# Performance work log

Measured on AMD Instinct MI355X. Metric: run time of the kernel, lower is better.

## Reference

```python
import jax, jax.numpy as jnp
import numpy as np

COMMITMENT_COST = 0.25
NUM_EMBEDDINGS = 8192
EMBED_DIM = 64


def setup_inputs() -> dict:
    key = jax.random.key(0)
    k1, k2 = jax.random.split(key)
    inputs = jax.random.normal(k1, (16, 32, 32, EMBED_DIM), dtype=jnp.float32)
    # nn.init.uniform_(-1/K, 1/K)
    codebook = jax.random.uniform(
        k2, (NUM_EMBEDDINGS, EMBED_DIM), dtype=jnp.float32,
        minval=-1.0 / NUM_EMBEDDINGS, maxval=1.0 / NUM_EMBEDDINGS)
    return {"inputs": inputs, "codebook": codebook}


def reference(inputs, codebook):
    D = codebook.shape[-1]
    flat = inputs.reshape(-1, D)  # [N, D]
    # Squared euclidean distances (same argmin as torch.cdist).
    d2 = (jnp.sum(flat * flat, axis=1, keepdims=True)
          - 2.0 * flat @ codebook.T
          + jnp.sum(codebook * codebook, axis=1))  # [N, K]
    idx = jnp.argmin(d2, axis=1)  # [N]
    # one-hot @ codebook == direct gather
    quantized = codebook[idx].reshape(inputs.shape)
    sg = jax.lax.stop_gradient
    e_latent = (sg(quantized) - inputs) ** 2
    q_latent = (quantized - sg(inputs)) ** 2
    loss = q_latent + COMMITMENT_COST * e_latent
    quantized_st = inputs + sg(quantized - inputs)  # straight-through
    return (loss, quantized_st)
```

## Files before the change

### kernel.cpp

```cpp
#include <hip/hip_runtime.h>
#include <float.h>

#define NROWS 16384
#define KC 8192
#define DIM 64
#define BM 128
#define KSPLIT 4
#define CPS (KC / KSPLIT)
#define TILE 256
#define NTILES (CPS / TILE)

typedef __attribute__((ext_vector_type(8))) short bf16x8;
typedef __attribute__((ext_vector_type(4))) float f32x4;

#define WS_CB16 0
#define WS_X16  (KC * DIM * 2)
#define WS_GMIN (WS_X16 + NROWS * DIM * 2)

__device__ inline unsigned short f2bf(float f) {
    union { float f; unsigned u; } v; v.f = f;
    unsigned u = v.u;
    unsigned r = u + 0x7FFFu + ((u >> 16) & 1u);
    return (unsigned short)(r >> 16);
}
__device__ inline unsigned asu(float f) { union { float f; unsigned u; } v; v.f = f; return v.u; }
__device__ inline float asf(unsigned u) { union { float f; unsigned u; } v; v.u = u; return v.f; }

__global__ __launch_bounds__(256) void vq_prep(
        const float* __restrict__ x, const float* __restrict__ cb,
        unsigned short* __restrict__ x16, unsigned short* __restrict__ cb16,
        unsigned* __restrict__ gmin) {
    const int bx = blockIdx.x;
    const int tid = threadIdx.x;
    if (bx < 512) {
        const int g = bx * 256 + tid;
        const float4* s = (const float4*)x + (size_t)g * 2;
        float4 a = s[0], b = s[1];
        bf16x8 o;
        o[0] = (short)f2bf(-a.x); o[1] = (short)f2bf(-a.y);
        o[2] = (short)f2bf(-a.z); o[3] = (short)f2bf(-a.w);
        o[4] = (short)f2bf(-b.x); o[5] = (short)f2bf(-b.y);
        o[6] = (short)f2bf(-b.z); o[7] = (short)f2bf(-b.w);
        ((bf16x8*)x16)[g] = o;
        if (g < NROWS) gmin[g] = 0xFFFFFFFFu;
    } else {
        const int g = (bx - 512) * 256 + tid;
        const float4* s = (const float4*)cb + (size_t)g * 2;
        float4 a = s[0], b = s[1];
        bf16x8 o;
        o[0] = (short)f2bf(a.x); o[1] = (short)f2bf(a.y);
        o[2] = (short)f2bf(a.z); o[3] = (short)f2bf(a.w);
        o[4] = (short)f2bf(b.x); o[5] = (short)f2bf(b.y);
        o[6] = (short)f2bf(b.z); o[7] = (short)f2bf(b.w);
        ((bf16x8*)cb16)[g] = o;
    }
}

__global__ __launch_bounds__(256, 2) void vq_main(
        const unsigned short* __restrict__ x16,
        const unsigned short* __restrict__ cb16,
        unsigned* __restrict__ gmin) {
    __shared__ __attribute__((aligned(16))) char smem[2][32768];

    const int tid = threadIdx.x;
    const int lane = tid & 63;
    const int wave = tid >> 6;
    const int waveM = wave >> 1, waveN = wave & 1;
    const int quad = lane >> 4, c15 = lane & 15;

    const int rowTile = blockIdx.x & 127;
    const int split = blockIdx.x >> 7;
    const int splitBase = split * CPS;
    const size_t rowBase = (size_t)rowTile * BM;

    unsigned srcOff[8], dstOff[8];
#pragma unroll
    for (int j = 0; j < 8; ++j) {
        int p = j * 256 + tid;
        int q = (p & ~7) | ((p & 7) ^ ((p >> 3) & 7));
        srcOff[j] = (unsigned)q * 16u;
        dstOff[j] = (unsigned)(j * 256 + wave * 64) * 16u;
    }
    const char* gcb = (const char*)cb16 + (size_t)splitBase * DIM * 2;

#pragma unroll
    for (int j = 0; j < 8; ++j)
        __builtin_amdgcn_global_load_lds(
            (const __attribute__((address_space(1))) void*)(gcb + srcOff[j]),
            (__attribute__((address_space(3))) void*)(&smem[0][0] + dstOff[j]),
            16, 0, 0);

    bf16x8 afr[4][2];
#pragma unroll
    for (int fm = 0; fm < 4; ++fm) {
        const unsigned short* xr = x16 + (rowBase + waveM * 64 + fm * 16 + c15) * DIM;
#pragma unroll
        for (int kk = 0; kk < 2; ++kk)
            afr[fm][kk] = *(const bf16x8*)(xr + kk * 32 + quad * 8);
    }

    float key[4][4];
#pragma unroll
    for (int a = 0; a < 4; ++a)
#pragma unroll
        for (int b = 0; b < 4; ++b) key[a][b] = FLT_MAX;
    unsigned slotReg[2][4];
#pragma unroll
    for (int h = 0; h < 2; ++h)
#pragma unroll
        for (int fnl = 0; fnl < 4; ++fnl)
            slotReg[h][fnl] = (unsigned)(splitBase + waveN * 128 + h * 64 +
                                         fnl * 16 + c15);
    const f32x4 Z = {0.f, 0.f, 0.f, 0.f};

    __syncthreads();

    for (int t = 0; t < NTILES; ++t) {
        const int buf = t & 1;
        if (t + 1 < NTILES) {
            const char* gn = gcb + (size_t)(t + 1) * TILE * DIM * 2;
            char* lb = &smem[buf ^ 1][0];
#pragma unroll
            for (int j = 0; j < 8; ++j)
                __builtin_amdgcn_global_load_lds(
                    (const __attribute__((address_space(1))) void*)(gn + srcOff[j]),
                    (__attribute__((address_space(3))) void*)(lb + dstOff[j]),
                    16, 0, 0);
        }

        const bf16x8* B16 = (const bf16x8*)&smem[buf][0];
#pragma unroll
        for (int h = 0; h < 2; ++h) {
            bf16x8 bfr[4][2];
#pragma unroll
            for (int fnl = 0; fnl < 4; ++fnl) {
                int rB = waveN * 128 + h * 64 + fnl * 16 + c15;
#pragma unroll
                for (int kk = 0; kk < 2; ++kk) {
                    int cch = kk * 4 + quad;
                    bfr[fnl][kk] = B16[rB * 8 + (cch ^ (rB & 7))];
                }
            }
            f32x4 acc[4][4];
#pragma unroll
            for (int fm = 0; fm < 4; ++fm)
#pragma unroll
                for (int fnl = 0; fnl < 4; ++fnl) {
                    f32x4 t0 = __builtin_amdgcn_mfma_f32_16x16x32_bf16(
                        afr[fm][0], bfr[fnl][0], Z, 0, 0, 0);
                    acc[fm][fnl] = __builtin_amdgcn_mfma_f32_16x16x32_bf16(
                        afr[fm][1], bfr[fnl][1], t0, 0, 0, 0);
                }
#pragma unroll
            for (int fm = 0; fm < 4; ++fm)
#pragma unroll
                for (int rg = 0; rg < 4; ++rg) {
                    unsigned u0 = (asu(acc[fm][0][rg]) & 0xFFFFE000u) | slotReg[h][0];
                    unsigned u1 = (asu(acc[fm][1][rg]) & 0xFFFFE000u) | slotReg[h][1];
                    unsigned u2 = (asu(acc[fm][2][rg]) & 0xFFFFE000u) | slotReg[h][2];
                    unsigned u3 = (asu(acc[fm][3][rg]) & 0xFFFFE000u) | slotReg[h][3];
                    float k = key[fm][rg];
                    k = fminf(k, fminf(asf(u0), asf(u1)));
                    k = fminf(k, fminf(asf(u2), asf(u3)));
                    key[fm][rg] = k;
                }
        }
#pragma unroll
        for (int h = 0; h < 2; ++h)
#pragma unroll
            for (int fnl = 0; fnl < 4; ++fnl) slotReg[h][fnl] += TILE;
        __syncthreads();
    }

#pragma unroll
    for (int fm = 0; fm < 4; ++fm)
#pragma unroll
        for (int rg = 0; rg < 4; ++rg) {
            float k = key[fm][rg];
            k = fminf(k, __shfl_xor(k, 1));
            k = fminf(k, __shfl_xor(k, 2));
            k = fminf(k, __shfl_xor(k, 4));
            k = fminf(k, __shfl_xor(k, 8));
            key[fm][rg] = k;
        }
    if (c15 == 0) {
#pragma unroll
        for (int fm = 0; fm < 4; ++fm)
#pragma unroll
            for (int rg = 0; rg < 4; ++rg) {
                unsigned u = asu(key[fm][rg]);
                unsigned m = (u & 0x80000000u) ? ~u : (u | 0x80000000u);
                atomicMin(&gmin[rowBase + waveM * 64 + fm * 16 + quad * 4 + rg], m);
            }
    }
}

__global__ __launch_bounds__(256) void vq_out(
        const float* __restrict__ x, const float* __restrict__ cb,
        const unsigned* __restrict__ gmin,
        float* __restrict__ out_loss, float* __restrict__ out_q) {
    __shared__ int idxs[16];
    const int tid = threadIdx.x;
    const size_t row0 = (size_t)blockIdx.x * 16;
    if (tid < 16) {
        unsigned u = gmin[row0 + tid];
        unsigned b = (u & 0x80000000u) ? (u ^ 0x80000000u) : ~u;
        idxs[tid] = (int)(b & 8191u);
    }
    __syncthreads();
    const int r = tid >> 4;
    const int d4 = tid & 15;
    const int code = idxs[r];
    float4 q4 = ((const float4*)(cb + (size_t)code * DIM))[d4];
    float4 x4 = ((const float4*)(x + (row0 + r) * DIM))[d4];
    float4 l4;
    l4.x = 1.25f * (q4.x - x4.x) * (q4.x - x4.x);
    l4.y = 1.25f * (q4.y - x4.y) * (q4.y - x4.y);
    l4.z = 1.25f * (q4.z - x4.z) * (q4.z - x4.z);
    l4.w = 1.25f * (q4.w - x4.w) * (q4.w - x4.w);
    ((float4*)out_loss)[(row0 + r) * 16 + d4] = l4;
    ((float4*)out_q)[(row0 + r) * 16 + d4] = q4;
}

extern "C" void kernel_launch(void* const* d_in, const int* in_sizes, int n_in,
                              void* d_out, int out_size, void* d_ws, size_t ws_size,
                              hipStream_t stream) {
    const float* x = (const float*)d_in[0];
    const float* cb = (const float*)d_in[1];
    char* ws = (char*)d_ws;
    unsigned short* cb16 = (unsigned short*)(ws + WS_CB16);
    unsigned short* x16 = (unsigned short*)(ws + WS_X16);
    unsigned* gmin = (unsigned*)(ws + WS_GMIN);

    float* out_loss = (float*)d_out;
    float* out_q = out_loss + (size_t)NROWS * DIM;

    vq_prep<<<768, 256, 0, stream>>>(x, cb, x16, cb16, gmin);
    vq_main<<<(NROWS / BM) * KSPLIT, 256, 0, stream>>>(x16, cb16, gmin);
    vq_out<<<NROWS / 16, 256, 0, stream>>>(x, cb, gmin, out_loss, out_q);
}
```

Before: 87.16 us.

## Fuse output gather into main kernel via last-block ticket and retile rows

Removes the separate output kernel: each row tile's split blocks atomically bump a counter, and the last arriving block reads the final argmin and writes loss and quantized outputs. Row tile shrinks to 64 and K-split drops to 2, so there are still 512 blocks, but each reuses a codebook tile over fewer rows. An in-block shared-memory reduction across the two N-waves now comes before the global atomicMin. This saves one kernel launch and a gmin round trip, but halves MFMA work per LDS codebook load and adds fences and atomics.

```diff
diff --git a/kernel.cpp b/kernel.cpp
--- a/kernel.cpp
+++ b/kernel.cpp
@@ -4,11 +4,12 @@
 #define NROWS 16384
 #define KC 8192
 #define DIM 64
-#define BM 128
-#define KSPLIT 4
+#define BM 64
+#define KSPLIT 2
 #define CPS (KC / KSPLIT)
 #define TILE 256
 #define NTILES (CPS / TILE)
+#define NRT (NROWS / BM)
 
 typedef __attribute__((ext_vector_type(8))) short bf16x8;
 typedef __attribute__((ext_vector_type(4))) float f32x4;
@@ -16,6 +17,7 @@
 #define WS_CB16 0
 #define WS_X16  (KC * DIM * 2)
 #define WS_GMIN (WS_X16 + NROWS * DIM * 2)
+#define WS_CNT  (WS_GMIN + NROWS * 4)
 
 __device__ inline unsigned short f2bf(float f) {
     union { float f; unsigned u; } v; v.f = f;
@@ -29,7 +31,7 @@
 __global__ __launch_bounds__(256) void vq_prep(
         const float* __restrict__ x, const float* __restrict__ cb,
         unsigned short* __restrict__ x16, unsigned short* __restrict__ cb16,
-        unsigned* __restrict__ gmin) {
+        unsigned* __restrict__ gmin, unsigned* __restrict__ cnt) {
     const int bx = blockIdx.x;
     const int tid = threadIdx.x;
     if (bx < 512) {
@@ -43,6 +45,7 @@
         o[6] = (short)f2bf(-b.z); o[7] = (short)f2bf(-b.w);
         ((bf16x8*)x16)[g] = o;
         if (g < NROWS) gmin[g] = 0xFFFFFFFFu;
+        if (g < NRT) cnt[g] = 0u;
     } else {
         const int g = (bx - 512) * 256 + tid;
         const float4* s = (const float4*)cb + (size_t)g * 2;
@@ -59,8 +62,13 @@
 __global__ __launch_bounds__(256, 2) void vq_main(
         const unsigned short* __restrict__ x16,
         const unsigned short* __restrict__ cb16,
-        unsigned* __restrict__ gmin) {
+        const float* __restrict__ x, const float* __restrict__ cb,
+        unsigned* __restrict__ gmin, unsigned* __restrict__ cnt,
+        float* __restrict__ out_loss, float* __restrict__ out_q) {
     __shared__ __attribute__((aligned(16))) char smem[2][32768];
+    __shared__ float redK[BM][2];
+    __shared__ int idxs[BM];
+    __shared__ int ticket;
 
     const int tid = threadIdx.x;
     const int lane = tid & 63;
@@ -68,8 +76,8 @@
     const int waveM = wave >> 1, waveN = wave & 1;
     const int quad = lane >> 4, c15 = lane & 15;
 
-    const int rowTile = blockIdx.x & 127;
-    const int split = blockIdx.x >> 7;
+    const int rowTile = blockIdx.x >> 1;
+    const int split = blockIdx.x & 1;
     const int splitBase = split * CPS;
     const size_t rowBase = (size_t)rowTile * BM;
 
@@ -90,18 +98,18 @@
             (__attribute__((address_space(3))) void*)(&smem[0][0] + dstOff[j]),
             16, 0, 0);
 
-    bf16x8 afr[4][2];
-#pragma unroll
-    for (int fm = 0; fm < 4; ++fm) {
-        const unsigned short* xr = x16 + (rowBase + waveM * 64 + fm * 16 + c15) * DIM;
+    bf16x8 afr[2][2];
+#pragma unroll
+    for (int fm = 0; fm < 2; ++fm) {
+        const unsigned short* xr = x16 + (rowBase + waveM * 32 + fm * 16 + c15) * DIM;
 #pragma unroll
         for (int kk = 0; kk < 2; ++kk)
             afr[fm][kk] = *(const bf16x8*)(xr + kk * 32 + quad * 8);
     }
 
-    float key[4][4];
-#pragma unroll
-    for (int a = 0; a < 4; ++a)
+    float key[2][4];
+#pragma unroll
+    for (int a = 0; a < 2; ++a)
 #pragma unroll
         for (int b = 0; b < 4; ++b) key[a][b] = FLT_MAX;
     unsigned slotReg[2][4];
@@ -141,9 +149,9 @@
                     bfr[fnl][kk] = B16[rB * 8 + (cch ^ (rB & 7))];
                 }
             }
-            f32x4 acc[4][4];
-#pragma unroll
-            for (int fm = 0; fm < 4; ++fm)
+            f32x4 acc[2][4];
+#pragma unroll
+            for (int fm = 0; fm < 2; ++fm)
 #pragma unroll
                 for (int fnl = 0; fnl < 4; ++fnl) {
                     f32x4 t0 = __builtin_amdgcn_mfma_f32_16x16x32_bf16(
@@ -152,7 +160,7 @@
                         afr[fm][1], bfr[fnl][1], t0, 0, 0, 0);
                 }
 #pragma unroll
-            for (int fm = 0; fm < 4; ++fm)
+            for (int fm = 0; fm < 2; ++fm)
 #pragma unroll
                 for (int rg = 0; rg < 4; ++rg) {
                     unsigned u0 = (asu(acc[fm][0][rg]) & 0xFFFFE000u) | slotReg[h][0];
@@ -173,7 +181,7 @@
     }
 
 #pragma unroll
-    for (int fm = 0; fm < 4; ++fm)
+    for (int fm = 0; fm < 2; ++fm)
 #pragma unroll
         for (int rg = 0; rg < 4; ++rg) {
             float k = key[fm][rg];
@@ -185,41 +193,49 @@
         }
     if (c15 == 0) {
 #pragma unroll
-        for (int fm = 0; fm < 4; ++fm)
-#pragma unroll
-            for (int rg = 0; rg < 4; ++rg) {
-                unsigned u = asu(key[fm][rg]);
-                unsigned m = (u & 0x80000000u) ? ~u : (u | 0x80000000u);
-                atomicMin(&gmin[rowBase + waveM * 64 + fm * 16 + quad * 4 + rg], m);
-            }
-    }
-}
-
-__global__ __launch_bounds__(256) void vq_out(
-        const float* __restrict__ x, const float* __restrict__ cb,
-        const unsigned* __restrict__ gmin,
-        float* __restrict__ out_loss, float* __restrict__ out_q) {
-    __shared__ int idxs[16];
-    const int tid = threadIdx.x;
-    const size_t row0 = (size_t)blockIdx.x * 16;
-    if (tid < 16) {
-        unsigned u = gmin[row0 + tid];
-        unsigned b = (u & 0x80000000u) ? (u ^ 0x80000000u) : ~u;
-        idxs[tid] = (int)(b & 8191u);
-    }
-    __syncthreads();
-    const int r = tid >> 4;
-    const int d4 = tid & 15;
-    const int code = idxs[r];
-    float4 q4 = ((const float4*)(cb + (size_t)code * DIM))[d4];
-    float4 x4 = ((const float4*)(x + (row0 + r) * DIM))[d4];
-    float4 l4;
-    l4.x = 1.25f * (q4.x - x4.x) * (q4.x - x4.x);
-    l4.y = 1.25f * (q4.y - x4.y) * (q4.y - x4.y);
-    l4.z = 1.25f * (q4.z - x4.z) * (q4.z - x4.z);
-    l4.w = 1.25f * (q4.w - x4.w) * (q4.w - x4.w);
-    ((float4*)out_loss)[(row0 + r) * 16 + d4] = l4;
-    ((float4*)out_q)[(row0 + r) * 16 + d4] = q4;
+        for (int fm = 0; fm < 2; ++fm)
+#pragma unroll
+            for (int rg = 0; rg < 4; ++rg)
+                redK[waveM * 32 + fm * 16 + quad * 4 + rg][waveN] = key[fm][rg];
+    }
+    __syncthreads();
+
+    if (tid < BM) {
+        float m = fminf(redK[tid][0], redK[tid][1]);
+        unsigned u = asu(m);
+        unsigned mp = (u & 0x80000000u) ? ~u : (u | 0x80000000u);
+        atomicMin(&gmin[rowBase + tid], mp);
+    }
+    __threadfence();
+    __syncthreads();
+    if (tid == 0) ticket = (int)atomicAdd(&cnt[rowTile], 1u);
+    __syncthreads();
+
+    if (ticket == KSPLIT - 1) {
+        __threadfence();
+        if (tid < BM) {
+            unsigned mm = atomicMin(&gmin[rowBase + tid], 0xFFFFFFFFu);
+            unsigned b = (mm & 0x80000000u) ? (mm ^ 0x80000000u) : ~mm;
+            idxs[tid] = (int)(b & 8191u);
+        }
+        __syncthreads();
+#pragma unroll
+        for (int j = 0; j < 4; ++j) {
+            int e = j * 256 + tid;
+            int r = e >> 4;
+            int d4 = e & 15;
+            int code = idxs[r];
+            float4 q4 = ((const float4*)(cb + (size_t)code * DIM))[d4];
+            float4 x4 = ((const float4*)(x + (rowBase + r) * DIM))[d4];
+            float4 l4;
+            l4.x = 1.25f * (q4.x - x4.x) * (q4.x - x4.x);
+            l4.y = 1.25f * (q4.y - x4.y) * (q4.y - x4.y);
+            l4.z = 1.25f * (q4.z - x4.z) * (q4.z - x4.z);
+            l4.w = 1.25f * (q4.w - x4.w) * (q4.w - x4.w);
+            ((float4*)out_loss)[(rowBase + r) * 16 + d4] = l4;
+            ((float4*)out_q)[(rowBase + r) * 16 + d4] = q4;
+        }
+    }
 }
 
 extern "C" void kernel_launch(void* const* d_in, const int* in_sizes, int n_in,
@@ -231,11 +247,12 @@
     unsigned short* cb16 = (unsigned short*)(ws + WS_CB16);
     unsigned short* x16 = (unsigned short*)(ws + WS_X16);
     unsigned* gmin = (unsigned*)(ws + WS_GMIN);
+    unsigned* cnt = (unsigned*)(ws + WS_CNT);
 
     float* out_loss = (float*)d_out;
     float* out_q = out_loss + (size_t)NROWS * DIM;
 
-    vq_prep<<<768, 256, 0, stream>>>(x, cb, x16, cb16, gmin);
-    vq_main<<<(NROWS / BM) * KSPLIT, 256, 0, stream>>>(x16, cb16, gmin);
-    vq_out<<<NROWS / 16, 256, 0, stream>>>(x, cb, gmin, out_loss, out_q);
-}
+    vq_prep<<<768, 256, 0, stream>>>(x, cb, x16, cb16, gmin, cnt);
+    vq_main<<<NRT * KSPLIT, 256, 0, stream>>>(x16, cb16, x, cb, gmin, cnt,
+                                              out_loss, out_q);
+}
```

Measured after the change: 134.6 us. 54.4% more time.

## Fuse prep, distance-argmin and output into one cooperative kernel with grid syncs

Applied to the files above, without the earlier changes.

Merges the three kernels into a single cooperative launch of 512 blocks that runs conversion, the MFMA distance/argmin, and the gather/loss phases separated by grid-wide syncs, with a fallback to three launches if the cooperative launch fails. To fit two blocks per CU with 32KB LDS, the codebook tile shrinks from 256 to 128 rows, and the block-to-tile mapping is interleaved across splits. The aim is to remove launch gaps between kernels. In exchange, grid.sync adds barrier cost, the smaller tile doubles loop iterations and syncthreads, and the output phase runs on fewer blocks.

```diff
diff --git a/kernel.cpp b/kernel.cpp
--- a/kernel.cpp
+++ b/kernel.cpp
@@ -1,5 +1,8 @@
 #include <hip/hip_runtime.h>
+#include <hip/hip_cooperative_groups.h>
 #include <float.h>
+
+namespace cg = cooperative_groups;
 
 #define NROWS 16384
 #define KC 8192
@@ -7,8 +10,9 @@
 #define BM 128
 #define KSPLIT 4
 #define CPS (KC / KSPLIT)
-#define TILE 256
+#define TILE 128
 #define NTILES (CPS / TILE)
+#define GRID 512
 
 typedef __attribute__((ext_vector_type(8))) short bf16x8;
 typedef __attribute__((ext_vector_type(4))) float f32x4;
@@ -26,14 +30,12 @@
 __device__ inline unsigned asu(float f) { union { float f; unsigned u; } v; v.f = f; return v.u; }
 __device__ inline float asf(unsigned u) { union { float f; unsigned u; } v; v.u = u; return v.f; }
 
-__global__ __launch_bounds__(256) void vq_prep(
+__device__ __forceinline__ void phaseA(int bx, int tid,
         const float* __restrict__ x, const float* __restrict__ cb,
         unsigned short* __restrict__ x16, unsigned short* __restrict__ cb16,
         unsigned* __restrict__ gmin) {
-    const int bx = blockIdx.x;
-    const int tid = threadIdx.x;
-    if (bx < 512) {
-        const int g = bx * 256 + tid;
+    const int g = bx * 256 + tid;
+    {
         const float4* s = (const float4*)x + (size_t)g * 2;
         float4 a = s[0], b = s[1];
         bf16x8 o;
@@ -42,9 +44,8 @@
         o[4] = (short)f2bf(-b.x); o[5] = (short)f2bf(-b.y);
         o[6] = (short)f2bf(-b.z); o[7] = (short)f2bf(-b.w);
         ((bf16x8*)x16)[g] = o;
-        if (g < NROWS) gmin[g] = 0xFFFFFFFFu;
-    } else {
-        const int g = (bx - 512) * 256 + tid;
+    }
+    if (g < KC * DIM / 8) {
         const float4* s = (const float4*)cb + (size_t)g * 2;
         float4 a = s[0], b = s[1];
         bf16x8 o;
@@ -54,28 +55,26 @@
         o[6] = (short)f2bf(b.z); o[7] = (short)f2bf(b.w);
         ((bf16x8*)cb16)[g] = o;
     }
-}
-
-__global__ __launch_bounds__(256, 2) void vq_main(
+    if (g < NROWS) gmin[g] = 0xFFFFFFFFu;
+}
+
+__device__ __forceinline__ void phaseB(int bx, int tid, char* smem,
         const unsigned short* __restrict__ x16,
         const unsigned short* __restrict__ cb16,
         unsigned* __restrict__ gmin) {
-    __shared__ __attribute__((aligned(16))) char smem[2][32768];
-
-    const int tid = threadIdx.x;
     const int lane = tid & 63;
     const int wave = tid >> 6;
     const int waveM = wave >> 1, waveN = wave & 1;
     const int quad = lane >> 4, c15 = lane & 15;
 
-    const int rowTile = blockIdx.x & 127;
-    const int split = blockIdx.x >> 7;
+    const int rowTile = bx >> 2;
+    const int split = bx & 3;
     const int splitBase = split * CPS;
     const size_t rowBase = (size_t)rowTile * BM;
 
-    unsigned srcOff[8], dstOff[8];
-#pragma unroll
-    for (int j = 0; j < 8; ++j) {
+    unsigned srcOff[4], dstOff[4];
+#pragma unroll
+    for (int j = 0; j < 4; ++j) {
         int p = j * 256 + tid;
         int q = (p & ~7) | ((p & 7) ^ ((p >> 3) & 7));
         srcOff[j] = (unsigned)q * 16u;
@@ -84,10 +83,10 @@
     const char* gcb = (const char*)cb16 + (size_t)splitBase * DIM * 2;
 
 #pragma unroll
-    for (int j = 0; j < 8; ++j)
+    for (int j = 0; j < 4; ++j)
         __builtin_amdgcn_global_load_lds(
             (const __attribute__((address_space(1))) void*)(gcb + srcOff[j]),
-            (__attribute__((address_space(3))) void*)(&smem[0][0] + dstOff[j]),
+            (__attribute__((address_space(3))) void*)(smem + dstOff[j]),
             16, 0, 0);
 
     bf16x8 afr[4][2];
@@ -104,13 +103,10 @@
     for (int a = 0; a < 4; ++a)
 #pragma unroll
         for (int b = 0; b < 4; ++b) key[a][b] = FLT_MAX;
-    unsigned slotReg[2][4];
-#pragma unroll
-    for (int h = 0; h < 2; ++h)
-#pragma unroll
-        for (int fnl = 0; fnl < 4; ++fnl)
-            slotReg[h][fnl] = (unsigned)(splitBase + waveN * 128 + h * 64 +
-                                         fnl * 16 + c15);
+    unsigned slotReg[4];
+#pragma unroll
+    for (int fnl = 0; fnl < 4; ++fnl)
+        slotReg[fnl] = (unsigned)(splitBase + waveN * 64 + fnl * 16 + c15);
     const f32x4 Z = {0.f, 0.f, 0.f, 0.f};
 
     __syncthreads();
@@ -119,56 +115,51 @@
         const int buf = t & 1;
         if (t + 1 < NTILES) {
             const char* gn = gcb + (size_t)(t + 1) * TILE * DIM * 2;
-            char* lb = &smem[buf ^ 1][0];
-#pragma unroll
-            for (int j = 0; j < 8; ++j)
+            char* lb = smem + (buf ^ 1) * 16384;
+#pragma unroll
+            for (int j = 0; j < 4; ++j)
                 __builtin_amdgcn_global_load_lds(
                     (const __attribute__((address_space(1))) void*)(gn + srcOff[j]),
                     (__attribute__((address_space(3))) void*)(lb + dstOff[j]),
                     16, 0, 0);
         }
 
-        const bf16x8* B16 = (const bf16x8*)&smem[buf][0];
-#pragma unroll
-        for (int h = 0; h < 2; ++h) {
-            bf16x8 bfr[4][2];
+        const bf16x8* B16 = (const bf16x8*)(smem + buf * 16384);
+        bf16x8 bfr[4][2];
+#pragma unroll
+        for (int fnl = 0; fnl < 4; ++fnl) {
+            int rB = waveN * 64 + fnl * 16 + c15;
+#pragma unroll
+            for (int kk = 0; kk < 2; ++kk) {
+                int cch = kk * 4 + quad;
+                bfr[fnl][kk] = B16[rB * 8 + (cch ^ (rB & 7))];
+            }
+        }
+        f32x4 acc[4][4];
+#pragma unroll
+        for (int fm = 0; fm < 4; ++fm)
 #pragma unroll
             for (int fnl = 0; fnl < 4; ++fnl) {
-                int rB = waveN * 128 + h * 64 + fnl * 16 + c15;
-#pragma unroll
-                for (int kk = 0; kk < 2; ++kk) {
-                    int cch = kk * 4 + quad;
-                    bfr[fnl][kk] = B16[rB * 8 + (cch ^ (rB & 7))];
-                }
-            }
-            f32x4 acc[4][4];
-#pragma unroll
-            for (int fm = 0; fm < 4; ++fm)
-#pragma unroll
-                for (int fnl = 0; fnl < 4; ++fnl) {
-                    f32x4 t0 = __builtin_amdgcn_mfma_f32_16x16x32_bf16(
-                        afr[fm][0], bfr[fnl][0], Z, 0, 0, 0);
-                    acc[fm][fnl] = __builtin_amdgcn_mfma_f32_16x16x32_bf16(
-                        afr[fm][1], bfr[fnl][1], t0, 0, 0, 0);
-                }
-#pragma unroll
-            for (int fm = 0; fm < 4; ++fm)
-#pragma unroll
-                for (int rg = 0; rg < 4; ++rg) {
-                    unsigned u0 = (asu(acc[fm][0][rg]) & 0xFFFFE000u) | slotReg[h][0];
-                    unsigned u1 = (asu(acc[fm][1][rg]) & 0xFFFFE000u) | slotReg[h][1];
-                    unsigned u2 = (asu(acc[fm][2][rg]) & 0xFFFFE000u) | slotReg[h][2];
-                    unsigned u3 = (asu(acc[fm][3][rg]) & 0xFFFFE000u) | slotReg[h][3];
-                    float k = key[fm][rg];
-                    k = fminf(k, fminf(asf(u0), asf(u1)));
-                    k = fminf(k, fminf(asf(u2), asf(u3)));
-                    key[fm][rg] = k;
-                }
-        }
-#pragma unroll
-        for (int h = 0; h < 2; ++h)
-#pragma unroll
-            for (int fnl = 0; fnl < 4; ++fnl) slotReg[h][fnl] += TILE;
+                f32x4 t0 = __builtin_amdgcn_mfma_f32_16x16x32_bf16(
+                    afr[fm][0], bfr[fnl][0], Z, 0, 0, 0);
+                acc[fm][fnl] = __builtin_amdgcn_mfma_f32_16x16x32_bf16(
+                    afr[fm][1], bfr[fnl][1], t0, 0, 0, 0);
+            }
+#pragma unroll
+        for (int fm = 0; fm < 4; ++fm)
+#pragma unroll
+            for (int rg = 0; rg < 4; ++rg) {
+                unsigned u0 = (asu(acc[fm][0][rg]) & 0xFFFFE000u) | slotReg[0];
+                unsigned u1 = (asu(acc[fm][1][rg]) & 0xFFFFE000u) | slotReg[1];
+                unsigned u2 = (asu(acc[fm][2][rg]) & 0xFFFFE000u) | slotReg[2];
+                unsigned u3 = (asu(acc[fm][3][rg]) & 0xFFFFE000u) | slotReg[3];
+                float k = key[fm][rg];
+                k = fminf(k, fminf(asf(u0), asf(u1)));
+                k = fminf(k, fminf(asf(u2), asf(u3)));
+                key[fm][rg] = k;
+            }
+#pragma unroll
+        for (int fnl = 0; fnl < 4; ++fnl) slotReg[fnl] += TILE;
         __syncthreads();
     }
 
@@ -195,31 +186,70 @@
     }
 }
 
-__global__ __launch_bounds__(256) void vq_out(
+__device__ __forceinline__ void phaseC(int bx, int tid, char* smem,
         const float* __restrict__ x, const float* __restrict__ cb,
         const unsigned* __restrict__ gmin,
         float* __restrict__ out_loss, float* __restrict__ out_q) {
-    __shared__ int idxs[16];
-    const int tid = threadIdx.x;
-    const size_t row0 = (size_t)blockIdx.x * 16;
-    if (tid < 16) {
+    int* idxs = (int*)smem;
+    const size_t row0 = (size_t)bx * 32;
+    if (tid < 32) {
         unsigned u = gmin[row0 + tid];
         unsigned b = (u & 0x80000000u) ? (u ^ 0x80000000u) : ~u;
         idxs[tid] = (int)(b & 8191u);
     }
     __syncthreads();
-    const int r = tid >> 4;
-    const int d4 = tid & 15;
-    const int code = idxs[r];
-    float4 q4 = ((const float4*)(cb + (size_t)code * DIM))[d4];
-    float4 x4 = ((const float4*)(x + (row0 + r) * DIM))[d4];
-    float4 l4;
-    l4.x = 1.25f * (q4.x - x4.x) * (q4.x - x4.x);
-    l4.y = 1.25f * (q4.y - x4.y) * (q4.y - x4.y);
-    l4.z = 1.25f * (q4.z - x4.z) * (q4.z - x4.z);
-    l4.w = 1.25f * (q4.w - x4.w) * (q4.w - x4.w);
-    ((float4*)out_loss)[(row0 + r) * 16 + d4] = l4;
-    ((float4*)out_q)[(row0 + r) * 16 + d4] = q4;
+#pragma unroll
+    for (int j = 0; j < 2; ++j) {
+        int e = j * 256 + tid;
+        int r = e >> 4;
+        int d4 = e & 15;
+        int code = idxs[r];
+        float4 q4 = ((const float4*)(cb + (size_t)code * DIM))[d4];
+        float4 x4 = ((const float4*)(x + (row0 + r) * DIM))[d4];
+        float4 l4;
+        l4.x = 1.25f * (q4.x - x4.x) * (q4.x - x4.x);
+        l4.y = 1.25f * (q4.y - x4.y) * (q4.y - x4.y);
+        l4.z = 1.25f * (q4.z - x4.z) * (q4.z - x4.z);
+        l4.w = 1.25f * (q4.w - x4.w) * (q4.w - x4.w);
+        ((float4*)out_loss)[(row0 + r) * 16 + d4] = l4;
+        ((float4*)out_q)[(row0 + r) * 16 + d4] = q4;
+    }
+}
+
+__global__ __launch_bounds__(256, 2) void vq_all(
+        const float* __restrict__ x, const float* __restrict__ cb,
+        unsigned short* __restrict__ x16, unsigned short* __restrict__ cb16,
+        unsigned* __restrict__ gmin,
+        float* __restrict__ out_loss, float* __restrict__ out_q) {
+    __shared__ __attribute__((aligned(16))) char smem[32768];
+    cg::grid_group grid = cg::this_grid();
+    const int bx = blockIdx.x, tid = threadIdx.x;
+
+    phaseA(bx, tid, x, cb, x16, cb16, gmin);
+    grid.sync();
+    phaseB(bx, tid, smem, x16, cb16, gmin);
+    grid.sync();
+    phaseC(bx, tid, smem, x, cb, gmin, out_loss, out_q);
+}
+
+__global__ __launch_bounds__(256) void vq_prepK(
+        const float* __restrict__ x, const float* __restrict__ cb,
+        unsigned short* __restrict__ x16, unsigned short* __restrict__ cb16,
+        unsigned* __restrict__ gmin) {
+    phaseA(blockIdx.x, threadIdx.x, x, cb, x16, cb16, gmin);
+}
+__global__ __launch_bounds__(256, 2) void vq_mainK(
+        const unsigned short* __restrict__ x16,
+        const unsigned short* __restrict__ cb16, unsigned* __restrict__ gmin) {
+    __shared__ __attribute__((aligned(16))) char smem[32768];
+    phaseB(blockIdx.x, threadIdx.x, smem, x16, cb16, gmin);
+}
+__global__ __launch_bounds__(256) void vq_outK(
+        const float* __restrict__ x, const float* __restrict__ cb,
+        const unsigned* __restrict__ gmin,
+        float* __restrict__ out_loss, float* __restrict__ out_q) {
+    __shared__ __attribute__((aligned(16))) char smem[256];
+    phaseC(blockIdx.x, threadIdx.x, smem, x, cb, gmin, out_loss, out_q);
 }
 
 extern "C" void kernel_launch(void* const* d_in, const int* in_sizes, int n_in,
@@ -235,7 +265,13 @@
     float* out_loss = (float*)d_out;
     float* out_q = out_loss + (size_t)NROWS * DIM;
 
-    vq_prep<<<768, 256, 0, stream>>>(x, cb, x16, cb16, gmin);
-    vq_main<<<(NROWS / BM) * KSPLIT, 256, 0, stream>>>(x16, cb16, gmin);
-    vq_out<<<NROWS / 16, 256, 0, stream>>>(x, cb, gmin, out_loss, out_q);
-}
+    void* args[] = {(void*)&x, (void*)&cb, (void*)&x16, (void*)&cb16,
+                    (void*)&gmin, (void*)&out_loss, (void*)&out_q};
+    hipError_t err = hipLaunchCooperativeKernel(
+        reinterpret_cast<void*>(vq_all), dim3(GRID), dim3(256), args, 0, stream);
+    if (err != hipSuccess) {
+        vq_prepK<<<GRID, 256, 0, stream>>>(x, cb, x16, cb16, gmin);
+        vq_mainK<<<GRID, 256, 0, stream>>>(x16, cb16, gmin);
+        vq_outK<<<GRID, 256, 0, stream>>>(x, cb, gmin, out_loss, out_q);
+    }
+}
```

Result: slower. 186.9 us (+114.5%).

## Pre-swizzle bf16 operands into MFMA fragment layout and drop LDS staging

Applied to the files above, without the earlier changes.

The prep kernel now writes x and the codebook in bf16 in an MFMA-fragment-major layout, so each lane loads its operand fragment with one coalesced 16-byte global load. The main kernel no longer stages codebook tiles through LDS with barriers. Instead each wave streams its own 1024 codes straight from global or L2 into registers, double-buffering fragments. The block index mapping is also changed so the four K-splits of a row tile run adjacently. This removes LDS traffic and __syncthreads, but each wave now reads its B fragments independently, so L2 traffic rises and global-load latency must be hidden by the register prefetch alone.

```diff
diff --git a/kernel.cpp b/kernel.cpp
--- a/kernel.cpp
+++ b/kernel.cpp
@@ -7,8 +7,9 @@
 #define BM 128
 #define KSPLIT 4
 #define CPS (KC / KSPLIT)
-#define TILE 256
-#define NTILES (CPS / TILE)
+#define NRT (NROWS / BM)
+#define GRID (NRT * KSPLIT)
+#define WITERS 16
 
 typedef __attribute__((ext_vector_type(8))) short bf16x8;
 typedef __attribute__((ext_vector_type(4))) float f32x4;
@@ -30,146 +31,114 @@
         const float* __restrict__ x, const float* __restrict__ cb,
         unsigned short* __restrict__ x16, unsigned short* __restrict__ cb16,
         unsigned* __restrict__ gmin) {
-    const int bx = blockIdx.x;
-    const int tid = threadIdx.x;
-    if (bx < 512) {
-        const int g = bx * 256 + tid;
-        const float4* s = (const float4*)x + (size_t)g * 2;
+    const int g = blockIdx.x * 256 + threadIdx.x;
+    {
+        const int r = g >> 3, p = g & 7;
+        const int kk = p >> 2, quad = p & 3;
+        const float4* s = (const float4*)(x + (size_t)r * DIM + kk * 32 + quad * 8);
         float4 a = s[0], b = s[1];
         bf16x8 o;
         o[0] = (short)f2bf(-a.x); o[1] = (short)f2bf(-a.y);
         o[2] = (short)f2bf(-a.z); o[3] = (short)f2bf(-a.w);
         o[4] = (short)f2bf(-b.x); o[5] = (short)f2bf(-b.y);
         o[6] = (short)f2bf(-b.z); o[7] = (short)f2bf(-b.w);
-        ((bf16x8*)x16)[g] = o;
-        if (g < NROWS) gmin[g] = 0xFFFFFFFFu;
-    } else {
-        const int g = (bx - 512) * 256 + tid;
-        const float4* s = (const float4*)cb + (size_t)g * 2;
+        const int dest = (((r >> 4) * 2 + kk) * 4 + quad) * 16 + (r & 15);
+        ((bf16x8*)x16)[dest] = o;
+    }
+    if (g < KC * DIM / 8) {
+        const int c = g >> 3, p = g & 7;
+        const int kk = p >> 2, quad = p & 3;
+        const float4* s = (const float4*)(cb + (size_t)c * DIM + kk * 32 + quad * 8);
         float4 a = s[0], b = s[1];
         bf16x8 o;
         o[0] = (short)f2bf(a.x); o[1] = (short)f2bf(a.y);
         o[2] = (short)f2bf(a.z); o[3] = (short)f2bf(a.w);
         o[4] = (short)f2bf(b.x); o[5] = (short)f2bf(b.y);
         o[6] = (short)f2bf(b.z); o[7] = (short)f2bf(b.w);
-        ((bf16x8*)cb16)[g] = o;
-    }
+        const int dest = (((c >> 4) * 2 + kk) * 4 + quad) * 16 + (c & 15);
+        ((bf16x8*)cb16)[dest] = o;
+    }
+    if (g < NROWS) gmin[g] = 0xFFFFFFFFu;
 }
 
 __global__ __launch_bounds__(256, 2) void vq_main(
         const unsigned short* __restrict__ x16,
         const unsigned short* __restrict__ cb16,
         unsigned* __restrict__ gmin) {
-    __shared__ __attribute__((aligned(16))) char smem[2][32768];
-
     const int tid = threadIdx.x;
     const int lane = tid & 63;
     const int wave = tid >> 6;
     const int waveM = wave >> 1, waveN = wave & 1;
     const int quad = lane >> 4, c15 = lane & 15;
 
-    const int rowTile = blockIdx.x & 127;
-    const int split = blockIdx.x >> 7;
+    const int rowTile = blockIdx.x >> 2;
+    const int split = blockIdx.x & 3;
     const int splitBase = split * CPS;
     const size_t rowBase = (size_t)rowTile * BM;
 
-    unsigned srcOff[8], dstOff[8];
-#pragma unroll
-    for (int j = 0; j < 8; ++j) {
-        int p = j * 256 + tid;
-        int q = (p & ~7) | ((p & 7) ^ ((p >> 3) & 7));
-        srcOff[j] = (unsigned)q * 16u;
-        dstOff[j] = (unsigned)(j * 256 + wave * 64) * 16u;
-    }
-    const char* gcb = (const char*)cb16 + (size_t)splitBase * DIM * 2;
-
-#pragma unroll
-    for (int j = 0; j < 8; ++j)
-        __builtin_amdgcn_global_load_lds(
-            (const __attribute__((address_space(1))) void*)(gcb + srcOff[j]),
-            (__attribute__((address_space(3))) void*)(&smem[0][0] + dstOff[j]),
-            16, 0, 0);
-
+    const bf16x8* X = (const bf16x8*)x16;
     bf16x8 afr[4][2];
 #pragma unroll
     for (int fm = 0; fm < 4; ++fm) {
-        const unsigned short* xr = x16 + (rowBase + waveM * 64 + fm * 16 + c15) * DIM;
+        const int rb = (int)(rowBase >> 4) + waveM * 4 + fm;
 #pragma unroll
         for (int kk = 0; kk < 2; ++kk)
-            afr[fm][kk] = *(const bf16x8*)(xr + kk * 32 + quad * 8);
-    }
+            afr[fm][kk] = X[(rb * 2 + kk) * 64 + lane];
+    }
+
+    const bf16x8* B = (const bf16x8*)cb16;
+    const int codeBase = splitBase + waveN * 1024;
+    const int cb0 = codeBase >> 4;
 
     float key[4][4];
 #pragma unroll
     for (int a = 0; a < 4; ++a)
 #pragma unroll
         for (int b = 0; b < 4; ++b) key[a][b] = FLT_MAX;
-    unsigned slotReg[2][4];
-#pragma unroll
-    for (int h = 0; h < 2; ++h)
-#pragma unroll
-        for (int fnl = 0; fnl < 4; ++fnl)
-            slotReg[h][fnl] = (unsigned)(splitBase + waveN * 128 + h * 64 +
-                                         fnl * 16 + c15);
     const f32x4 Z = {0.f, 0.f, 0.f, 0.f};
 
-    __syncthreads();
-
-    for (int t = 0; t < NTILES; ++t) {
-        const int buf = t & 1;
-        if (t + 1 < NTILES) {
-            const char* gn = gcb + (size_t)(t + 1) * TILE * DIM * 2;
-            char* lb = &smem[buf ^ 1][0];
-#pragma unroll
-            for (int j = 0; j < 8; ++j)
-                __builtin_amdgcn_global_load_lds(
-                    (const __attribute__((address_space(1))) void*)(gn + srcOff[j]),
-                    (__attribute__((address_space(3))) void*)(lb + dstOff[j]),
-                    16, 0, 0);
+    bf16x8 bfr[2][4][2];
+#pragma unroll
+    for (int fn = 0; fn < 4; ++fn)
+#pragma unroll
+        for (int kk = 0; kk < 2; ++kk)
+            bfr[0][fn][kk] = B[((cb0 + fn) * 2 + kk) * 64 + lane];
+
+#pragma unroll
+    for (int it = 0; it < WITERS; ++it) {
+        const int cur = it & 1;
+        if (it + 1 < WITERS) {
+            const int cbn = cb0 + (it + 1) * 4;
+#pragma unroll
+            for (int fn = 0; fn < 4; ++fn)
+#pragma unroll
+                for (int kk = 0; kk < 2; ++kk)
+                    bfr[cur ^ 1][fn][kk] = B[((cbn + fn) * 2 + kk) * 64 + lane];
         }
-
-        const bf16x8* B16 = (const bf16x8*)&smem[buf][0];
-#pragma unroll
-        for (int h = 0; h < 2; ++h) {
-            bf16x8 bfr[4][2];
-#pragma unroll
-            for (int fnl = 0; fnl < 4; ++fnl) {
-                int rB = waveN * 128 + h * 64 + fnl * 16 + c15;
-#pragma unroll
-                for (int kk = 0; kk < 2; ++kk) {
-                    int cch = kk * 4 + quad;
-                    bfr[fnl][kk] = B16[rB * 8 + (cch ^ (rB & 7))];
-                }
+        f32x4 acc[4][4];
+#pragma unroll
+        for (int fm = 0; fm < 4; ++fm)
+#pragma unroll
+            for (int fn = 0; fn < 4; ++fn) {
+                f32x4 t0 = __builtin_amdgcn_mfma_f32_16x16x32_bf16(
+                    afr[fm][0], bfr[cur][fn][0], Z, 0, 0, 0);
+                acc[fm][fn] = __builtin_amdgcn_mfma_f32_16x16x32_bf16(
+                    afr[fm][1], bfr[cur][fn][1], t0, 0, 0, 0);
             }
-            f32x4 acc[4][4];
-#pragma unroll
-            for (int fm = 0; fm < 4; ++fm)
-#pragma unroll
-                for (int fnl = 0; fnl < 4; ++fnl) {
-                    f32x4 t0 = __builtin_amdgcn_mfma_f32_16x16x32_bf16(
-                        afr[fm][0], bfr[fnl][0], Z, 0, 0, 0);
-                    acc[fm][fnl] = __builtin_amdgcn_mfma_f32_16x16x32_bf16(
-                        afr[fm][1], bfr[fnl][1], t0, 0, 0, 0);
-                }
-#pragma unroll
-            for (int fm = 0; fm < 4; ++fm)
-#pragma unroll
-                for (int rg = 0; rg < 4; ++rg) {
-                    unsigned u0 = (asu(acc[fm][0][rg]) & 0xFFFFE000u) | slotReg[h][0];
-                    unsigned u1 = (asu(acc[fm][1][rg]) & 0xFFFFE000u) | slotReg[h][1];
-                    unsigned u2 = (asu(acc[fm][2][rg]) & 0xFFFFE000u) | slotReg[h][2];
-                    unsigned u3 = (asu(acc[fm][3][rg]) & 0xFFFFE000u) | slotReg[h][3];
-                    float k = key[fm][rg];
-                    k = fminf(k, fminf(asf(u0), asf(u1)));
-                    k = fminf(k, fminf(asf(u2), asf(u3)));
-                    key[fm][rg] = k;
-                }
-        }
-#pragma unroll
-        for (int h = 0; h < 2; ++h)
-#pragma unroll
-            for (int fnl = 0; fnl < 4; ++fnl) slotReg[h][fnl] += TILE;
-        __syncthreads();
+        const unsigned s0 = (unsigned)(codeBase + it * 64 + c15);
+#pragma unroll
+        for (int fm = 0; fm < 4; ++fm)
+#pragma unroll
+            for (int rg = 0; rg < 4; ++rg) {
+                unsigned u0 = (asu(acc[fm][0][rg]) & 0xFFFFE000u) | (s0);
+                unsigned u1 = (asu(acc[fm][1][rg]) & 0xFFFFE000u) | (s0 + 16);
+                unsigned u2 = (asu(acc[fm][2][rg]) & 0xFFFFE000u) | (s0 + 32);
+                unsigned u3 = (asu(acc[fm][3][rg]) & 0xFFFFE000u) | (s0 + 48);
+                float k = key[fm][rg];
+                k = fminf(k, fminf(asf(u0), asf(u1)));
+                k = fminf(k, fminf(asf(u2), asf(u3)));
+                key[fm][rg] = k;
+            }
     }
 
 #pragma unroll
@@ -235,7 +204,7 @@
     float* out_loss = (float*)d_out;
     float* out_q = out_loss + (size_t)NROWS * DIM;
 
-    vq_prep<<<768, 256, 0, stream>>>(x, cb, x16, cb16, gmin);
-    vq_main<<<(NROWS / BM) * KSPLIT, 256, 0, stream>>>(x16, cb16, gmin);
+    vq_prep<<<GRID, 256, 0, stream>>>(x, cb, x16, cb16, gmin);
+    vq_main<<<GRID, 256, 0, stream>>>(x16, cb16, gmin);
     vq_out<<<NROWS / 16, 256, 0, stream>>>(x, cb, gmin, out_loss, out_q);
 }
```

Measured after the change: 86.21 us. About the same (-1.1%).
